# Kernel optimization log

Measured on AMD Instinct MI355X. Metric: run time of the kernel, lower is better.

The kernel has to match this reference:

```python
import jax, jax.numpy as jnp
import numpy as np

# Dims implied by init: input_dim=128, b_dim=64 -> per-branch Mamba d_model=16
D_MODEL = 16
D_STATE = 16
D_CONV = 4
D_INNER = 32   # expand * d_model
DT_RANK = 1    # ceil(d_model / 16)
EPS = 1e-5


def _ln(x, g, b):
    m = x.mean(-1, keepdims=True)
    v = x.var(-1, keepdims=True)
    return (x - m) / jnp.sqrt(v + EPS) * g + b


def _gn(x, g, b, groups):
    B, C, H, W = x.shape
    xr = x.reshape(B, groups, C // groups, H, W)
    m = xr.mean((2, 3, 4), keepdims=True)
    v = xr.var((2, 3, 4), keepdims=True)
    xr = (xr - m) / jnp.sqrt(v + EPS)
    return xr.reshape(B, C, H, W) * g[None, :, None, None] + b[None, :, None, None]


def _mamba(u, in_proj_w, conv_w, conv_b, x_proj_w, dt_proj_w, dt_proj_b, A_log, Dp, out_proj_w):
    # u: [N, L, d_model]
    N, L, _ = u.shape
    xz = u @ in_proj_w.T                       # [N, L, 2*d_inner]
    xc, zg = jnp.split(xz, 2, axis=-1)
    # causal depthwise conv1d over L
    xt = xc.transpose(0, 2, 1)                 # [N, d_inner, L]
    xt = jax.lax.conv_general_dilated(
        xt, conv_w, (1,), [(D_CONV - 1, 0)],
        dimension_numbers=('NCH', 'OIH', 'NCH'),
        feature_group_count=D_INNER)
    xt = xt + conv_b[None, :, None]
    xc = jax.nn.silu(xt).transpose(0, 2, 1)    # [N, L, d_inner]
    x_dbl = xc @ x_proj_w.T                    # [N, L, dt_rank + 2*d_state]
    dt = x_dbl[..., :DT_RANK]
    Bv = x_dbl[..., DT_RANK:DT_RANK + D_STATE]
    Cv = x_dbl[..., DT_RANK + D_STATE:]
    dt = jax.nn.softplus(dt @ dt_proj_w.T + dt_proj_b)  # [N, L, d_inner]
    A = -jnp.exp(A_log)                        # [d_inner, d_state]

    def step(h, inp):
        dt_t, B_t, C_t, x_t = inp              # [N,di],[N,ds],[N,ds],[N,di]
        dA = jnp.exp(dt_t[:, :, None] * A)     # [N, di, ds]
        h = dA * h + (dt_t * x_t)[:, :, None] * B_t[:, None, :]
        y = jnp.einsum('nds,ns->nd', h, C_t)
        return h, y

    h0 = jnp.zeros((N, D_INNER, D_STATE), u.dtype)
    xs = (dt.transpose(1, 0, 2), Bv.transpose(1, 0, 2),
          Cv.transpose(1, 0, 2), xc.transpose(1, 0, 2))
    _, ys = jax.lax.scan(step, h0, xs)         # ys: [L, N, d_inner]
    y = ys.transpose(1, 0, 2) + xc * Dp        # skip via D
    y = y * jax.nn.silu(zg)
    return y @ out_proj_w.T                    # [N, L, d_model]


def _forward(x, pre_ln_g, pre_ln_b, bott_in_w, bott_in_b,
             in_proj_w, conv_w, conv_b, x_proj_w, dt_proj_w, dt_proj_b,
             A_log, Dp, out_proj_w, post_ln_g, post_ln_b,
             bott_out_w, bott_out_b, res_scale,
             fc1_w, gn1_g, gn1_b, fc2_w, gn2_g, gn2_b):
    B, C, H, W = x.shape
    L = H * W
    # ---- PVMLayer token mixer ----
    xf = x.reshape(B, C, L).transpose(0, 2, 1)            # [B, L, C]
    z = _ln(xf, pre_ln_g, pre_ln_b)
    z = z @ bott_in_w.T + bott_in_b                       # [B, L, 64]
    # four chunks share the same Mamba weights -> batch them together
    zc = z.reshape(B, L, 4, D_MODEL).transpose(2, 0, 1, 3).reshape(4 * B, L, D_MODEL)
    m = _mamba(zc, in_proj_w, conv_w, conv_b, x_proj_w, dt_proj_w, dt_proj_b,
               A_log, Dp, out_proj_w) + zc
    z = m.reshape(4, B, L, D_MODEL).transpose(1, 2, 0, 3).reshape(B, L, 4 * D_MODEL)
    z = _ln(z, post_ln_g, post_ln_b)
    z = (z @ bott_out_w.T + bott_out_b) * res_scale       # [B, L, C]
    token = z.transpose(0, 2, 1).reshape(B, C, H, W)
    mixed = x + token                                     # PVMLayer residual (eval: drop_path=id)
    out = x + mixed                                       # PVMFormer residual
    # ---- Mlp (1x1 conv + GroupNorm) ----
    h = jnp.einsum('bchw,oc->bohw', out, fc1_w)
    h = _gn(h, gn1_g, gn1_b, 32)
    h = jax.nn.gelu(h, approximate=False)
    h = jnp.einsum('bchw,oc->bohw', h, fc2_w)
    h = _gn(h, gn2_g, gn2_b, 32)
    return out + h


def setup_inputs() -> dict:
    key = jax.random.key(0)
    ks = jax.random.split(key, 16)
    n = lambda k, s, sc=0.02: jax.random.normal(k, s, jnp.float32) * sc
    C = 128
    return {
        'x': jax.random.normal(ks[0], (8, C, 64, 64), jnp.float32),
        'pre_ln_g': jnp.ones((C,), jnp.float32),
        'pre_ln_b': jnp.zeros((C,), jnp.float32),
        'bott_in_w': n(ks[1], (64, C)),
        'bott_in_b': jnp.zeros((64,), jnp.float32),
        'in_proj_w': n(ks[2], (2 * D_INNER, D_MODEL)),
        'conv_w': n(ks[3], (D_INNER, 1, D_CONV), 0.1),
        'conv_b': jnp.zeros((D_INNER,), jnp.float32),
        'x_proj_w': n(ks[4], (DT_RANK + 2 * D_STATE, D_INNER)),
        'dt_proj_w': n(ks[5], (D_INNER, DT_RANK), 0.5),
        'dt_proj_b': n(ks[6], (D_INNER,), 0.5),
        'A_log': jnp.log(jnp.broadcast_to(jnp.arange(1.0, D_STATE + 1.0, dtype=jnp.float32), (D_INNER, D_STATE))),
        'Dp': jnp.ones((D_INNER,), jnp.float32),
        'out_proj_w': n(ks[7], (D_MODEL, D_INNER)),
        'post_ln_g': jnp.ones((64,), jnp.float32),
        'post_ln_b': jnp.zeros((64,), jnp.float32),
        'bott_out_w': n(ks[8], (C, 64)),
        'bott_out_b': jnp.zeros((C,), jnp.float32),
        'res_scale': jnp.array(0.5, jnp.float32),
        'fc1_w': n(ks[9], (4 * C, C)),
        'gn1_g': jnp.ones((4 * C,), jnp.float32),
        'gn1_b': jnp.zeros((4 * C,), jnp.float32),
        'fc2_w': n(ks[10], (C, 4 * C)),
        'gn2_g': jnp.ones((C,), jnp.float32),
        'gn2_b': jnp.zeros((C,), jnp.float32),
    }


def reference(x, pre_ln_g, pre_ln_b, bott_in_w, bott_in_b,
              in_proj_w, conv_w, conv_b, x_proj_w, dt_proj_w, dt_proj_b,
              A_log, Dp, out_proj_w, post_ln_g, post_ln_b,
              bott_out_w, bott_out_b, res_scale,
              fc1_w, gn1_g, gn1_b, fc2_w, gn2_g, gn2_b):
    return _forward(x, pre_ln_g, pre_ln_b, bott_in_w, bott_in_b,
                    in_proj_w, conv_w, conv_b, x_proj_w, dt_proj_w, dt_proj_b,
                    A_log, Dp, out_proj_w, post_ln_g, post_ln_b,
                    bott_out_w, bott_out_b, res_scale,
                    fc1_w, gn1_g, gn1_b, fc2_w, gn2_g, gn2_b)
```

## Files before the change

kernel.cpp:

```cpp
#include <hip/hip_runtime.h>
#include <hip/hip_bf16.h>
#include <math.h>

#define L4K 4096
#define NCH 32
#define CL  128
#define TB  32
#define NST (CL/TB)

typedef __attribute__((ext_vector_type(8))) short short8;
typedef __attribute__((ext_vector_type(4))) float f32x4;

__device__ __forceinline__ unsigned short f2b(float f) {
    unsigned int u = __float_as_uint(f);
    unsigned int r = u + 0x7FFFu + ((u >> 16) & 1u);
    return (unsigned short)(r >> 16);
}
__device__ __forceinline__ float b2f(unsigned short h) {
    return __uint_as_float(((unsigned int)h) << 16);
}

__global__ __launch_bounds__(256) void k1_pre(
    const float* __restrict__ x, const float* __restrict__ png, const float* __restrict__ pnb,
    const float* __restrict__ biw, const float* __restrict__ bib, const float* __restrict__ ipw,
    float* __restrict__ zc, float* __restrict__ xcp, float* __restrict__ zg)
{
    __shared__ float xs[128*32];
    __shared__ float wl[64*128];
    __shared__ float zs[32*65];
    __shared__ float ipl[64*16];
    __shared__ float pngs[128], pnbs[128];
    int tid = threadIdx.x;
    int l0 = blockIdx.x*32, b = blockIdx.y;
    const float* xb = x + (size_t)b*128*L4K;
    for (int it = 0; it < 16; ++it) {
        int f = it*256 + tid; int c = f>>5, i = f&31;
        xs[f] = xb[(size_t)c*L4K + l0 + i];
    }
    for (int f = tid; f < 8192; f += 256) wl[f] = biw[f];
    for (int f = tid; f < 1024; f += 256) ipl[f] = ipw[f];
    if (tid < 128) { pngs[tid] = png[tid]; pnbs[tid] = pnb[tid]; }
    __syncthreads();
    int i = tid & 31, q = tid >> 5;
    float s = 0.f, s2 = 0.f;
    for (int c = 0; c < 128; ++c) { float v = xs[c*32+i]; s += v; s2 = fmaf(v,v,s2); }
    float mn = s*(1.f/128.f);
    float rstd = rsqrtf(s2*(1.f/128.f) - mn*mn + 1e-5f);
    float z[8];
    #pragma unroll
    for (int jj = 0; jj < 8; ++jj) z[jj] = bib[q*8+jj];
    for (int c = 0; c < 128; ++c) {
        float xv = (xs[c*32+i] - mn)*rstd*pngs[c] + pnbs[c];
        #pragma unroll
        for (int jj = 0; jj < 8; ++jj) z[jj] = fmaf(xv, wl[(q*8+jj)*128 + c], z[jj]);
    }
    #pragma unroll
    for (int jj = 0; jj < 8; ++jj) zs[i*65 + q*8 + jj] = z[jj];
    __syncthreads();
    if (tid < 128) {
        int i2 = tid & 31, g = tid >> 5;
        int n = g*8 + b; int l = l0 + i2;
        float zv[16];
        #pragma unroll
        for (int k = 0; k < 16; ++k) zv[k] = zs[i2*65 + g*16 + k];
        size_t tb = (size_t)n*L4K + l;
        float4* zc4 = (float4*)(zc + tb*16);
        zc4[0] = make_float4(zv[0],zv[1],zv[2],zv[3]);
        zc4[1] = make_float4(zv[4],zv[5],zv[6],zv[7]);
        zc4[2] = make_float4(zv[8],zv[9],zv[10],zv[11]);
        zc4[3] = make_float4(zv[12],zv[13],zv[14],zv[15]);
        float* xo = xcp + tb*32;
        float* zo = zg + tb*32;
        #pragma unroll
        for (int o = 0; o < 64; ++o) {
            float a = 0.f;
            #pragma unroll
            for (int k = 0; k < 16; ++k) a = fmaf(zv[k], ipl[o*16+k], a);
            if (o < 32) xo[o] = a; else zo[o-32] = a;
        }
    }
}

__global__ __launch_bounds__(128) void k2_conv(
    const float* __restrict__ xcp, const float* __restrict__ cw, const float* __restrict__ cb,
    const float* __restrict__ xpw, const float* __restrict__ dtw, const float* __restrict__ dtb,
    float* __restrict__ S)
{
    __shared__ float xt[131*33];
    __shared__ float cwl[128], cbl[32], xpl[33*32], dtwl[32], dtbl[32];
    int tid = threadIdx.x;
    int t0 = blockIdx.x*128; int n = blockIdx.y;
    const float* xb = xcp + (size_t)n*L4K*32;
    for (int f = tid; f < 131*32; f += 128) {
        int r = f >> 5, d = f & 31;
        int t = t0 - 3 + r;
        xt[r*33 + d] = (t >= 0) ? xb[(size_t)t*32 + d] : 0.f;
    }
    if (tid < 128) cwl[tid] = cw[tid];
    if (tid < 32) { cbl[tid] = cb[tid]; dtwl[tid] = dtw[tid]; dtbl[tid] = dtb[tid]; }
    for (int f = tid; f < 33*32; f += 128) xpl[f] = xpw[f];
    __syncthreads();
    int t = t0 + tid;
    float xc[32];
    #pragma unroll
    for (int d = 0; d < 32; ++d) {
        float sv = cbl[d];
        #pragma unroll
        for (int k = 0; k < 4; ++k) sv = fmaf(cwl[d*4+k], xt[(tid+k)*33 + d], sv);
        xc[d] = sv / (1.f + __expf(-sv));
    }
    float dtr = 0.f; float Bv[16], Cv[16];
    #pragma unroll
    for (int dd = 0; dd < 32; ++dd) dtr = fmaf(xc[dd], xpl[dd], dtr);
    #pragma unroll
    for (int o = 0; o < 16; ++o) {
        float a = 0.f, a2 = 0.f;
        #pragma unroll
        for (int dd = 0; dd < 32; ++dd) {
            a  = fmaf(xc[dd], xpl[(1+o)*32+dd],  a);
            a2 = fmaf(xc[dd], xpl[(17+o)*32+dd], a2);
        }
        Bv[o] = a; Cv[o] = a2;
    }
    float* r = S + ((size_t)n*L4K + t)*128;
    #pragma unroll
    for (int d = 0; d < 32; ++d) {
        float dv = fmaf(dtr, dtwl[d], dtbl[d]);
        float sp = fmaxf(dv, 0.f) + log1pf(__expf(-fabsf(dv)));
        r[d]      = sp;
        r[32 + d] = sp * xc[d];
        r[96 + d] = xc[d];
    }
    #pragma unroll
    for (int o = 0; o < 16; ++o) { r[64+o] = Bv[o]; r[80+o] = Cv[o]; }
}

__global__ __launch_bounds__(512) void k3a_local(
    const float* __restrict__ S, const float* __restrict__ alog,
    float* __restrict__ chunkA, float* __restrict__ chunkH)
{
    __shared__ float sb[2][TB*128];
    int tid = threadIdx.x;
    int d = tid >> 4, s = tid & 15;
    int chunk = blockIdx.x, n = blockIdx.y;
    float A = -__expf(alog[d*16 + s]);
    const float4* Sg = (const float4*)(S + ((size_t)n*L4K + (size_t)chunk*CL)*128);
    float4 p0 = Sg[tid], p1 = Sg[tid + 512];
    ((float4*)sb[0])[tid] = p0; ((float4*)sb[0])[tid+512] = p1;
    __syncthreads();
    float h = 0.f, ap = 1.f;
    for (int st = 0; st < NST; ++st) {
        int cur = st & 1;
        float4 q0, q1;
        if (st+1 < NST) {
            const float4* Sn = Sg + (size_t)(st+1)*TB*32;
            q0 = Sn[tid]; q1 = Sn[tid+512];
        }
        const float* sc = sb[cur];
        #pragma unroll
        for (int tl = 0; tl < TB; ++tl) {
            float dtv = sc[tl*128 + d];
            float dxv = sc[tl*128 + 32 + d];
            float Bvv = sc[tl*128 + 64 + s];
            float dA = __expf(dtv * A);
            h = fmaf(dA, h, dxv * Bvv);
            ap *= dA;
        }
        if (st+1 < NST) {
            ((float4*)sb[cur^1])[tid] = q0;
            ((float4*)sb[cur^1])[tid+512] = q1;
            __syncthreads();
        }
    }
    chunkA[(size_t)chunk*16384 + n*512 + tid] = ap;
    chunkH[(size_t)chunk*16384 + n*512 + tid] = h;
}

__global__ __launch_bounds__(256) void k3b_prefix(
    const float* __restrict__ chunkA, const float* __restrict__ chunkH,
    float* __restrict__ hstart)
{
    int nds = blockIdx.x*256 + threadIdx.x;
    float h = 0.f;
    hstart[nds] = 0.f;
    for (int c = 0; c < NCH-1; ++c) {
        h = fmaf(h, chunkA[(size_t)c*16384 + nds], chunkH[(size_t)c*16384 + nds]);
        hstart[(size_t)(c+1)*16384 + nds] = h;
    }
}

__global__ __launch_bounds__(512) void k3c_emit(
    const float* __restrict__ S, const float* __restrict__ alog,
    const float* __restrict__ hstart, float* __restrict__ y)
{
    __shared__ float sb[2][TB*128];
    __shared__ float ys[TB*32];
    int tid = threadIdx.x;
    int d = tid >> 4, s = tid & 15;
    int chunk = blockIdx.x, n = blockIdx.y;
    float A = -__expf(alog[d*16 + s]);
    const float4* Sg = (const float4*)(S + ((size_t)n*L4K + (size_t)chunk*CL)*128);
    float4* yg = (float4*)(y + ((size_t)n*L4K + (size_t)chunk*CL)*32);
    float4 p0 = Sg[tid], p1 = Sg[tid + 512];
    ((float4*)sb[0])[tid] = p0; ((float4*)sb[0])[tid+512] = p1;
    float h = hstart[(size_t)chunk*16384 + n*512 + tid];
    __syncthreads();
    for (int st = 0; st < NST; ++st) {
        int cur = st & 1;
        float4 q0, q1;
        if (st+1 < NST) {
            const float4* Sn = Sg + (size_t)(st+1)*TB*32;
            q0 = Sn[tid]; q1 = Sn[tid+512];
        }
        const float* sc = sb[cur];
        #pragma unroll
        for (int tl = 0; tl < TB; ++tl) {
            float dtv = sc[tl*128 + d];
            float dxv = sc[tl*128 + 32 + d];
            float Bvv = sc[tl*128 + 64 + s];
            float Cvv = sc[tl*128 + 80 + s];
            float dA = __expf(dtv * A);
            h = fmaf(dA, h, dxv * Bvv);
            float p = h * Cvv;
            p += __shfl_xor(p, 8, 16);
            p += __shfl_xor(p, 4, 16);
            p += __shfl_xor(p, 2, 16);
            p += __shfl_xor(p, 1, 16);
            if (s == 0) ys[tl*32 + d] = p;
        }
        if (st+1 < NST) {
            ((float4*)sb[cur^1])[tid] = q0;
            ((float4*)sb[cur^1])[tid+512] = q1;
        }
        __syncthreads();
        if (tid < TB*8) yg[(size_t)st*TB*8 + tid] = ((const float4*)ys)[tid];
        __syncthreads();
    }
}

__global__ __launch_bounds__(256) void k5_out(
    const float* __restrict__ y, const float* __restrict__ S, const float* __restrict__ zg,
    const float* __restrict__ zc, const float* __restrict__ Dp, const float* __restrict__ opw,
    float* __restrict__ m)
{
    int id = blockIdx.x*256 + threadIdx.x;
    int n = id >> 12, t = id & 4095;
    const float* yp  = y  + (size_t)id*32;
    const float* xcr = S  + (size_t)id*128 + 96;
    const float* zgp = zg + (size_t)id*32;
    const float* zcp = zc + (size_t)id*16;
    float v[32];
    #pragma unroll
    for (int dd = 0; dd < 32; ++dd) {
        float g = zgp[dd];
        float sig = 1.f/(1.f + __expf(-g));
        v[dd] = (yp[dd] + xcr[dd]*Dp[dd]) * (g*sig);
    }
    int b = n & 7, g4 = n >> 3;
    float* mp = m + ((size_t)b*L4K + t)*64 + g4*16;
    #pragma unroll
    for (int j = 0; j < 16; ++j) {
        float a = zcp[j];
        #pragma unroll
        for (int dd = 0; dd < 32; ++dd) a = fmaf(v[dd], opw[j*32+dd], a);
        mp[j] = a;
    }
}

__global__ __launch_bounds__(256) void k6_post(
    const float* __restrict__ m, const float* __restrict__ x,
    const float* __restrict__ pog, const float* __restrict__ pob,
    const float* __restrict__ bow, const float* __restrict__ bob,
    const float* __restrict__ rsp, float* __restrict__ outp,
    unsigned short* __restrict__ outpb)
{
    __shared__ float ms[64*65];
    __shared__ float wl[128*64];
    __shared__ float pogs[64], pobs[64];
    int tid = threadIdx.x;
    int l0 = blockIdx.x*64, b = blockIdx.y;
    const float* mb = m + ((size_t)b*L4K + l0)*64;
    for (int f = tid; f < 4096; f += 256) {
        int i = f>>6, j = f&63;
        ms[i*65 + j] = mb[f];
    }
    for (int f = tid; f < 8192; f += 256) wl[f] = bow[f];
    if (tid < 64) { pogs[tid] = pog[tid]; pobs[tid] = pob[tid]; }
    __syncthreads();
    float rs = rsp[0];
    int i = tid & 63, q = tid >> 6;
    float s = 0.f, s2 = 0.f;
    for (int j = 0; j < 64; ++j) { float v = ms[i*65+j]; s += v; s2 = fmaf(v,v,s2); }
    float mn = s*(1.f/64.f);
    float rstd = rsqrtf(s2*(1.f/64.f) - mn*mn + 1e-5f);
    float acc[32];
    #pragma unroll
    for (int cc = 0; cc < 32; ++cc) acc[cc] = bob[q*32+cc];
    for (int j = 0; j < 64; ++j) {
        float v = (ms[i*65+j]-mn)*rstd*pogs[j] + pobs[j];
        #pragma unroll
        for (int cc = 0; cc < 32; ++cc) acc[cc] = fmaf(v, wl[(q*32+cc)*64+j], acc[cc]);
    }
    const float* xb = x + (size_t)b*128*L4K + l0 + i;
    float* ob = outp + (size_t)b*128*L4K + l0 + i;
    unsigned short pk[32];
    #pragma unroll
    for (int cc = 0; cc < 32; ++cc) {
        int c = q*32 + cc;
        float val = 2.f*xb[(size_t)c*L4K] + acc[cc]*rs;
        ob[(size_t)c*L4K] = val;
        pk[cc] = f2b(val);
    }
    uint4* op = (uint4*)&outpb[((size_t)b*L4K + l0 + i)*128 + q*32];
    #pragma unroll
    for (int u = 0; u < 4; ++u) {
        uint4 v;
        v.x = pk[u*8+0] | ((unsigned)pk[u*8+1]<<16);
        v.y = pk[u*8+2] | ((unsigned)pk[u*8+3]<<16);
        v.z = pk[u*8+4] | ((unsigned)pk[u*8+5]<<16);
        v.w = pk[u*8+6] | ((unsigned)pk[u*8+7]<<16);
        op[u] = v;
    }
}

template<int KCHUNKS, bool OUT_BF16>
__global__ __launch_bounds__(256) void gemm_mfma(
    const unsigned short* __restrict__ Ab, const float* __restrict__ Wg,
    void* __restrict__ Dout, int Kpitch, int Npitch)
{
    __shared__ char lds[65536];
    int tid = threadIdx.x;
    int lane = tid & 63, w = tid >> 6;
    int l0 = blockIdx.x * 128, n0 = blockIdx.y * 128, b = blockIdx.z;
    size_t arow0 = (size_t)b*L4K + l0;
    int wm = (w>>1)*64, wn = (w&1)*64;
    f32x4 acc[4][4] = {};
    char* aL = lds;
    char* wL = lds + 32768;
    for (int kc = 0; kc < KCHUNKS; ++kc) {
        if (kc) __syncthreads();
        #pragma unroll
        for (int it = 0; it < 8; ++it) {
            int f = it*256 + tid;
            int row = f >> 4, kp = f & 15;
            uint4 v = *(const uint4*)&Ab[(arow0 + row)*(size_t)Kpitch + kc*128 + kp*8];
            int off = row*256 + kp*16; off ^= (row&7)<<4;
            *(uint4*)(aL + off) = v;
        }
        #pragma unroll
        for (int it = 0; it < 16; ++it) {
            int f = it*256 + tid;
            int row = f >> 5, kg = f & 31;
            float4 v = *(const float4*)&Wg[(size_t)(n0+row)*(KCHUNKS*128) + kc*128 + kg*4];
            uint2 p;
            p.x = f2b(v.x) | ((unsigned)f2b(v.y)<<16);
            p.y = f2b(v.z) | ((unsigned)f2b(v.w)<<16);
            int off = row*256 + kg*8; off ^= (row&7)<<4;
            *(uint2*)(wL + off) = p;
        }
        __syncthreads();
        #pragma unroll
        for (int ks = 0; ks < 4; ++ks) {
            short8 af[4], wf[4];
            int kb = ks*64 + (lane>>4)*16;
            #pragma unroll
            for (int mi = 0; mi < 4; ++mi) {
                int row = wm + mi*16 + (lane&15);
                int off = row*256 + kb; off ^= (row&7)<<4;
                af[mi] = *(const short8*)(aL + off);
            }
            #pragma unroll
            for (int ni = 0; ni < 4; ++ni) {
                int row = wn + ni*16 + (lane&15);
                int off = row*256 + kb; off ^= (row&7)<<4;
                wf[ni] = *(const short8*)(wL + off);
            }
            #pragma unroll
            for (int mi = 0; mi < 4; ++mi)
                #pragma unroll
                for (int ni = 0; ni < 4; ++ni)
                    acc[mi][ni] = __builtin_amdgcn_mfma_f32_16x16x32_bf16(af[mi], wf[ni], acc[mi][ni], 0, 0, 0);
        }
    }
    if (OUT_BF16) {
        __syncthreads();
        unsigned short* cL = (unsigned short*)lds;
        #pragma unroll
        for (int mi = 0; mi < 4; ++mi)
            #pragma unroll
            for (int ni = 0; ni < 4; ++ni)
                #pragma unroll
                for (int r = 0; r < 4; ++r) {
                    int row = wm + mi*16 + (lane>>4)*4 + r;
                    int col = wn + ni*16 + (lane&15);
                    cL[row*136 + col] = f2b(acc[mi][ni][r]);
                }
        __syncthreads();
        unsigned short* D = (unsigned short*)Dout;
        #pragma unroll
        for (int it = 0; it < 8; ++it) {
            int f = it*256 + tid;
            int row = f >> 4, kp = f & 15;
            uint4 v = *(const uint4*)&cL[row*136 + kp*8];
            *(uint4*)&D[(arow0 + row)*(size_t)Npitch + n0 + kp*8] = v;
        }
    } else {
        float* D = (float*)Dout;
        #pragma unroll
        for (int mi = 0; mi < 4; ++mi)
            #pragma unroll
            for (int ni = 0; ni < 4; ++ni)
                #pragma unroll
                for (int r = 0; r < 4; ++r) {
                    int row = wm + mi*16 + (lane>>4)*4 + r;
                    int col = wn + ni*16 + (lane&15);
                    D[(arow0 + row)*(size_t)Npitch + n0 + col] = acc[mi][ni][r];
                }
    }
}

__global__ __launch_bounds__(256) void k_gn1stats(
    const unsigned short* __restrict__ h, float* __restrict__ stats)
{
    __shared__ float sred[256], sred2[256];
    int tid = threadIdx.x;
    int b = blockIdx.x >> 5, g = blockIdx.x & 31;
    float s = 0.f, s2 = 0.f;
    for (int it = 0; it < 32; ++it) {
        int f = it*256 + tid;
        int l = f >> 1, half = f & 1;
        uint4 v = *(const uint4*)&h[((size_t)b*L4K + l)*512 + g*16 + half*8];
        unsigned int ws[4] = {v.x, v.y, v.z, v.w};
        #pragma unroll
        for (int u = 0; u < 4; ++u) {
            float a = b2f((unsigned short)(ws[u] & 0xFFFF));
            float c = b2f((unsigned short)(ws[u] >> 16));
            s += a + c; s2 = fmaf(a,a,s2); s2 = fmaf(c,c,s2);
        }
    }
    sred[tid] = s; sred2[tid] = s2; __syncthreads();
    for (int off = 128; off; off >>= 1) {
        if (tid < off) { sred[tid] += sred[tid+off]; sred2[tid] += sred2[tid+off]; }
        __syncthreads();
    }
    if (tid == 0) {
        float inv = 1.f/65536.f;
        float mn = sred[0]*inv;
        float var = sred2[0]*inv - mn*mn;
        stats[blockIdx.x*2]   = mn;
        stats[blockIdx.x*2+1] = rsqrtf(var + 1e-5f);
    }
}

__global__ __launch_bounds__(256) void k9_gngelu(
    unsigned short* __restrict__ h, const float* __restrict__ stats,
    const float* __restrict__ g1, const float* __restrict__ b1)
{
    size_t idx = ((size_t)blockIdx.x*256 + threadIdx.x)*8;
    int o0 = (int)(idx & 511);
    int b = (int)(idx >> 21);
    int sg = b*32 + (o0 >> 4);
    float mn = stats[sg*2], rstd = stats[sg*2+1];
    uint4 v = *(uint4*)&h[idx];
    unsigned int ws[4] = {v.x, v.y, v.z, v.w};
    unsigned int out[4];
    #pragma unroll
    for (int u = 0; u < 4; ++u) {
        float a = b2f((unsigned short)(ws[u] & 0xFFFF));
        float c = b2f((unsigned short)(ws[u] >> 16));
        int o = o0 + u*2;
        float ta = (a-mn)*rstd*g1[o]   + b1[o];
        float tc = (c-mn)*rstd*g1[o+1] + b1[o+1];
        ta = 0.5f*ta*(1.f + erff(ta*0.70710678118654752f));
        tc = 0.5f*tc*(1.f + erff(tc*0.70710678118654752f));
        out[u] = f2b(ta) | ((unsigned)f2b(tc)<<16);
    }
    uint4 r; r.x = out[0]; r.y = out[1]; r.z = out[2]; r.w = out[3];
    *(uint4*)&h[idx] = r;
}

__global__ __launch_bounds__(256) void k_gn2stats(
    const float* __restrict__ h, float* __restrict__ stats)
{
    __shared__ float sred[256], sred2[256];
    int tid = threadIdx.x;
    int b = blockIdx.x >> 5, g = blockIdx.x & 31;
    float s = 0.f, s2 = 0.f;
    for (int it = 0; it < 16; ++it) {
        int l = it*256 + tid;
        float4 v = ((const float4*)h)[((size_t)b*L4K + l)*32 + g];
        s += v.x+v.y+v.z+v.w;
        s2 = fmaf(v.x,v.x,s2); s2 = fmaf(v.y,v.y,s2); s2 = fmaf(v.z,v.z,s2); s2 = fmaf(v.w,v.w,s2);
    }
    sred[tid] = s; sred2[tid] = s2; __syncthreads();
    for (int off = 128; off; off >>= 1) {
        if (tid < off) { sred[tid] += sred[tid+off]; sred2[tid] += sred2[tid+off]; }
        __syncthreads();
    }
    if (tid == 0) {
        float inv = 1.f/16384.f;
        float mn = sred[0]*inv;
        float var = sred2[0]*inv - mn*mn;
        stats[blockIdx.x*2]   = mn;
        stats[blockIdx.x*2+1] = rsqrtf(var + 1e-5f);
    }
}

__global__ __launch_bounds__(256) void k12_final(
    const float* __restrict__ outp, const float* __restrict__ h2t,
    const float* __restrict__ stats, const float* __restrict__ g2,
    const float* __restrict__ b2, float* __restrict__ out)
{
    __shared__ float T[32*33];
    int tid = threadIdx.x;
    int l0 = blockIdx.x*32, c0 = blockIdx.y*32, b = blockIdx.z;
    {
        int i = tid >> 3, jq = tid & 7;
        float4 v = ((const float4*)h2t)[((size_t)b*L4K + l0 + i)*32 + (c0>>2) + jq];
        int sg = b*32 + (c0>>2) + jq;
        float mn = stats[sg*2], rstd = stats[sg*2+1];
        int c = c0 + jq*4;
        T[(jq*4+0)*33 + i] = (v.x-mn)*rstd*g2[c+0] + b2[c+0];
        T[(jq*4+1)*33 + i] = (v.y-mn)*rstd*g2[c+1] + b2[c+1];
        T[(jq*4+2)*33 + i] = (v.z-mn)*rstd*g2[c+2] + b2[c+2];
        T[(jq*4+3)*33 + i] = (v.w-mn)*rstd*g2[c+3] + b2[c+3];
    }
    __syncthreads();
    {
        int c = tid >> 3, iq = tid & 7;
        size_t gi = ((size_t)b*128 + c0 + c)*1024 + (l0>>2) + iq;
        float4 o = ((const float4*)outp)[gi];
        float4 r;
        r.x = o.x + T[c*33 + iq*4 + 0];
        r.y = o.y + T[c*33 + iq*4 + 1];
        r.z = o.z + T[c*33 + iq*4 + 2];
        r.w = o.w + T[c*33 + iq*4 + 3];
        ((float4*)out)[gi] = r;
    }
}

extern "C" void kernel_launch(void* const* d_in, const int* in_sizes, int n_in,
                              void* d_out, int out_size, void* d_ws, size_t ws_size,
                              hipStream_t stream) {
    (void)in_sizes; (void)n_in; (void)out_size; (void)ws_size;
    const float* x    = (const float*)d_in[0];
    const float* png  = (const float*)d_in[1];
    const float* pnb  = (const float*)d_in[2];
    const float* biw  = (const float*)d_in[3];
    const float* bib  = (const float*)d_in[4];
    const float* ipw  = (const float*)d_in[5];
    const float* cw   = (const float*)d_in[6];
    const float* cb   = (const float*)d_in[7];
    const float* xpw  = (const float*)d_in[8];
    const float* dtw  = (const float*)d_in[9];
    const float* dtb  = (const float*)d_in[10];
    const float* alog = (const float*)d_in[11];
    const float* Dp   = (const float*)d_in[12];
    const float* opw  = (const float*)d_in[13];
    const float* pog  = (const float*)d_in[14];
    const float* pob  = (const float*)d_in[15];
    const float* bow  = (const float*)d_in[16];
    const float* bob  = (const float*)d_in[17];
    const float* rsp  = (const float*)d_in[18];
    const float* f1w  = (const float*)d_in[19];
    const float* g1g  = (const float*)d_in[20];
    const float* g1b  = (const float*)d_in[21];
    const float* f2w  = (const float*)d_in[22];
    const float* g2g  = (const float*)d_in[23];
    const float* g2b  = (const float*)d_in[24];

    char* ws = (char*)d_ws;
    float* S    = (float*)(ws + 0);
    float* zc   = (float*)(ws + 67108864);
    float* zg   = (float*)(ws + 75497472);
    float* xcp  = (float*)(ws + 92274688);
    float* y    = (float*)(ws + 92274688);
    float* m    = (float*)(ws + 109051904);
    float* chA  = (float*)(ws + 109051904);
    float* chH  = (float*)(ws + 109051904 + 2097152);
    float* hst  = (float*)(ws + 109051904 + 4194304);
    float*          outp  = (float*)(ws + 0);
    unsigned short* outpb = (unsigned short*)(ws + 16777216);
    unsigned short* h1tb  = (unsigned short*)(ws + 25165824);
    float*          h2t   = (float*)(ws + 58720256);
    float*          st1   = (float*)(ws + 75497472);
    float*          st2   = (float*)(ws + 75501568);

    k1_pre<<<dim3(128,8),256,0,stream>>>(x,png,pnb,biw,bib,ipw,zc,xcp,zg);
    k2_conv<<<dim3(32,32),128,0,stream>>>(xcp,cw,cb,xpw,dtw,dtb,S);
    k3a_local<<<dim3(NCH,32),512,0,stream>>>(S,alog,chA,chH);
    k3b_prefix<<<64,256,0,stream>>>(chA,chH,hst);
    k3c_emit<<<dim3(NCH,32),512,0,stream>>>(S,alog,hst,y);
    k5_out<<<512,256,0,stream>>>(y,S,zg,zc,Dp,opw,m);
    k6_post<<<dim3(64,8),256,0,stream>>>(m,x,pog,pob,bow,bob,rsp,outp,outpb);
    gemm_mfma<1,true><<<dim3(32,4,8),256,0,stream>>>(outpb,f1w,(void*)h1tb,128,512);
    k_gn1stats<<<256,256,0,stream>>>(h1tb,st1);
    k9_gngelu<<<8192,256,0,stream>>>(h1tb,st1,g1g,g1b);
    gemm_mfma<4,false><<<dim3(32,1,8),256,0,stream>>>(h1tb,f2w,(void*)h2t,512,128);
    k_gn2stats<<<256,256,0,stream>>>(h2t,st2);
    k12_final<<<dim3(128,4,8),256,0,stream>>>(outp,h2t,st2,g2g,g2b,(float*)d_out);
}
```

Baseline: 476.5 us.

## Switch intermediates to channel-major layout and stream scan inputs from global memory

Intermediate buffers (zc, xcp, zg, S, y, m) are stored channel-major, [n][channel][time], instead of time-major, so per-thread time-indexed accesses coalesce across threads. The chunked scan kernels drop their LDS double-buffering and instead read float4 runs of time steps directly from global memory, with a one-step register prefetch. The emit kernel replaces its shuffle reduction with a DPP row reduction and writes y straight out. The risk is that each thread now streams its own strided rows, relying on cache hits for the redundant B/C reads across d, and that k1's scattered writes become more strided.

```diff
diff --git a/kernel.cpp b/kernel.cpp
--- a/kernel.cpp
+++ b/kernel.cpp
@@ -5,8 +5,7 @@
 #define L4K 4096
 #define NCH 32
 #define CL  128
-#define TB  32
-#define NST (CL/TB)
+#define SPN (128*4096)
 
 typedef __attribute__((ext_vector_type(8))) short short8;
 typedef __attribute__((ext_vector_type(4))) float f32x4;
@@ -18,6 +17,18 @@
 }
 __device__ __forceinline__ float b2f(unsigned short h) {
     return __uint_as_float(((unsigned int)h) << 16);
+}
+__device__ __forceinline__ float rowsum16(float p) {
+    int t;
+    t = __builtin_amdgcn_update_dpp(0, __float_as_int(p), 0x128, 0xf, 0xf, false);
+    p += __int_as_float(t);
+    t = __builtin_amdgcn_update_dpp(0, __float_as_int(p), 0x124, 0xf, 0xf, false);
+    p += __int_as_float(t);
+    t = __builtin_amdgcn_update_dpp(0, __float_as_int(p), 0x122, 0xf, 0xf, false);
+    p += __int_as_float(t);
+    t = __builtin_amdgcn_update_dpp(0, __float_as_int(p), 0x121, 0xf, 0xf, false);
+    p += __int_as_float(t);
+    return p;
 }
 
 __global__ __launch_bounds__(256) void k1_pre(
@@ -63,20 +74,17 @@
         float zv[16];
         #pragma unroll
         for (int k = 0; k < 16; ++k) zv[k] = zs[i2*65 + g*16 + k];
-        size_t tb = (size_t)n*L4K + l;
-        float4* zc4 = (float4*)(zc + tb*16);
-        zc4[0] = make_float4(zv[0],zv[1],zv[2],zv[3]);
-        zc4[1] = make_float4(zv[4],zv[5],zv[6],zv[7]);
-        zc4[2] = make_float4(zv[8],zv[9],zv[10],zv[11]);
-        zc4[3] = make_float4(zv[12],zv[13],zv[14],zv[15]);
-        float* xo = xcp + tb*32;
-        float* zo = zg + tb*32;
+        float* zcb = zc + ((size_t)n*16)*L4K + l;
+        #pragma unroll
+        for (int k = 0; k < 16; ++k) zcb[(size_t)k*L4K] = zv[k];
+        float* xo = xcp + ((size_t)n*32)*L4K + l;
+        float* zo = zg  + ((size_t)n*32)*L4K + l;
         #pragma unroll
         for (int o = 0; o < 64; ++o) {
             float a = 0.f;
             #pragma unroll
             for (int k = 0; k < 16; ++k) a = fmaf(zv[k], ipl[o*16+k], a);
-            if (o < 32) xo[o] = a; else zo[o-32] = a;
+            if (o < 32) xo[(size_t)o*L4K] = a; else zo[(size_t)(o-32)*L4K] = a;
         }
     }
 }
@@ -90,11 +98,15 @@
     __shared__ float cwl[128], cbl[32], xpl[33*32], dtwl[32], dtbl[32];
     int tid = threadIdx.x;
     int t0 = blockIdx.x*128; int n = blockIdx.y;
-    const float* xb = xcp + (size_t)n*L4K*32;
-    for (int f = tid; f < 131*32; f += 128) {
-        int r = f >> 5, d = f & 31;
-        int t = t0 - 3 + r;
-        xt[r*33 + d] = (t >= 0) ? xb[(size_t)t*32 + d] : 0.f;
+    const float* xb = xcp + (size_t)n*32*L4K;
+    #pragma unroll 4
+    for (int d = 0; d < 32; ++d) {
+        int t = t0 - 3 + tid;
+        xt[tid*33 + d] = (t >= 0) ? xb[(size_t)d*L4K + t] : 0.f;
+        if (tid < 3) {
+            int r = 128 + tid; int t2 = t0 - 3 + r;
+            xt[r*33 + d] = xb[(size_t)d*L4K + t2];
+        }
     }
     if (tid < 128) cwl[tid] = cw[tid];
     if (tid < 32) { cbl[tid] = cb[tid]; dtwl[tid] = dtw[tid]; dtbl[tid] = dtb[tid]; }
@@ -122,58 +134,49 @@
         }
         Bv[o] = a; Cv[o] = a2;
     }
-    float* r = S + ((size_t)n*L4K + t)*128;
+    float* Sn = S + (size_t)n*SPN + t;
     #pragma unroll
     for (int d = 0; d < 32; ++d) {
         float dv = fmaf(dtr, dtwl[d], dtbl[d]);
         float sp = fmaxf(dv, 0.f) + log1pf(__expf(-fabsf(dv)));
-        r[d]      = sp;
-        r[32 + d] = sp * xc[d];
-        r[96 + d] = xc[d];
-    }
-    #pragma unroll
-    for (int o = 0; o < 16; ++o) { r[64+o] = Bv[o]; r[80+o] = Cv[o]; }
+        Sn[(size_t)d*L4K]      = sp;
+        Sn[(size_t)(32+d)*L4K] = sp * xc[d];
+        Sn[(size_t)(96+d)*L4K] = xc[d];
+    }
+    #pragma unroll
+    for (int o = 0; o < 16; ++o) {
+        Sn[(size_t)(64+o)*L4K] = Bv[o];
+        Sn[(size_t)(80+o)*L4K] = Cv[o];
+    }
 }
 
 __global__ __launch_bounds__(512) void k3a_local(
     const float* __restrict__ S, const float* __restrict__ alog,
     float* __restrict__ chunkA, float* __restrict__ chunkH)
 {
-    __shared__ float sb[2][TB*128];
     int tid = threadIdx.x;
     int d = tid >> 4, s = tid & 15;
     int chunk = blockIdx.x, n = blockIdx.y;
     float A = -__expf(alog[d*16 + s]);
-    const float4* Sg = (const float4*)(S + ((size_t)n*L4K + (size_t)chunk*CL)*128);
-    float4 p0 = Sg[tid], p1 = Sg[tid + 512];
-    ((float4*)sb[0])[tid] = p0; ((float4*)sb[0])[tid+512] = p1;
-    __syncthreads();
+    const float* base = S + (size_t)n*SPN + (size_t)chunk*CL;
+    const float4* pdt = (const float4*)(base + (size_t)d*L4K);
+    const float4* pdx = (const float4*)(base + (size_t)(32+d)*L4K);
+    const float4* pB  = (const float4*)(base + (size_t)(64+s)*L4K);
+    float4 cdt = pdt[0], cdx = pdx[0], cB = pB[0];
     float h = 0.f, ap = 1.f;
-    for (int st = 0; st < NST; ++st) {
-        int cur = st & 1;
-        float4 q0, q1;
-        if (st+1 < NST) {
-            const float4* Sn = Sg + (size_t)(st+1)*TB*32;
-            q0 = Sn[tid]; q1 = Sn[tid+512];
-        }
-        const float* sc = sb[cur];
-        #pragma unroll
-        for (int tl = 0; tl < TB; ++tl) {
-            float dtv = sc[tl*128 + d];
-            float dxv = sc[tl*128 + 32 + d];
-            float Bvv = sc[tl*128 + 64 + s];
-            float dA = __expf(dtv * A);
-            h = fmaf(dA, h, dxv * Bvv);
-            ap *= dA;
-        }
-        if (st+1 < NST) {
-            ((float4*)sb[cur^1])[tid] = q0;
-            ((float4*)sb[cur^1])[tid+512] = q1;
-            __syncthreads();
-        }
-    }
-    chunkA[(size_t)chunk*16384 + n*512 + tid] = ap;
-    chunkH[(size_t)chunk*16384 + n*512 + tid] = h;
+    #define A_STEP(c1,c2,c3) { float dA = __expf(c1*A); h = fmaf(dA, h, c2*c3); ap *= dA; }
+    for (int i = 0; i < CL/4 - 1; ++i) {
+        float4 ndt = pdt[i+1], ndx = pdx[i+1], nB = pB[i+1];
+        A_STEP(cdt.x, cdx.x, cB.x) A_STEP(cdt.y, cdx.y, cB.y)
+        A_STEP(cdt.z, cdx.z, cB.z) A_STEP(cdt.w, cdx.w, cB.w)
+        cdt = ndt; cdx = ndx; cB = nB;
+    }
+    A_STEP(cdt.x, cdx.x, cB.x) A_STEP(cdt.y, cdx.y, cB.y)
+    A_STEP(cdt.z, cdx.z, cB.z) A_STEP(cdt.w, cdx.w, cB.w)
+    #undef A_STEP
+    size_t idx = (size_t)chunk*16384 + n*512 + tid;
+    chunkA[idx] = ap;
+    chunkH[idx] = h;
 }
 
 __global__ __launch_bounds__(256) void k3b_prefix(
@@ -193,49 +196,38 @@
     const float* __restrict__ S, const float* __restrict__ alog,
     const float* __restrict__ hstart, float* __restrict__ y)
 {
-    __shared__ float sb[2][TB*128];
-    __shared__ float ys[TB*32];
     int tid = threadIdx.x;
     int d = tid >> 4, s = tid & 15;
     int chunk = blockIdx.x, n = blockIdx.y;
     float A = -__expf(alog[d*16 + s]);
-    const float4* Sg = (const float4*)(S + ((size_t)n*L4K + (size_t)chunk*CL)*128);
-    float4* yg = (float4*)(y + ((size_t)n*L4K + (size_t)chunk*CL)*32);
-    float4 p0 = Sg[tid], p1 = Sg[tid + 512];
-    ((float4*)sb[0])[tid] = p0; ((float4*)sb[0])[tid+512] = p1;
+    const float* base = S + (size_t)n*SPN + (size_t)chunk*CL;
+    const float4* pdt = (const float4*)(base + (size_t)d*L4K);
+    const float4* pdx = (const float4*)(base + (size_t)(32+d)*L4K);
+    const float4* pB  = (const float4*)(base + (size_t)(64+s)*L4K);
+    const float4* pC  = (const float4*)(base + (size_t)(80+s)*L4K);
+    float4* yb = (float4*)(y + ((size_t)n*32 + d)*L4K + (size_t)chunk*CL);
+    float4 cdt = pdt[0], cdx = pdx[0], cB = pB[0], cC = pC[0];
     float h = hstart[(size_t)chunk*16384 + n*512 + tid];
-    __syncthreads();
-    for (int st = 0; st < NST; ++st) {
-        int cur = st & 1;
-        float4 q0, q1;
-        if (st+1 < NST) {
-            const float4* Sn = Sg + (size_t)(st+1)*TB*32;
-            q0 = Sn[tid]; q1 = Sn[tid+512];
-        }
-        const float* sc = sb[cur];
-        #pragma unroll
-        for (int tl = 0; tl < TB; ++tl) {
-            float dtv = sc[tl*128 + d];
-            float dxv = sc[tl*128 + 32 + d];
-            float Bvv = sc[tl*128 + 64 + s];
-            float Cvv = sc[tl*128 + 80 + s];
-            float dA = __expf(dtv * A);
-            h = fmaf(dA, h, dxv * Bvv);
-            float p = h * Cvv;
-            p += __shfl_xor(p, 8, 16);
-            p += __shfl_xor(p, 4, 16);
-            p += __shfl_xor(p, 2, 16);
-            p += __shfl_xor(p, 1, 16);
-            if (s == 0) ys[tl*32 + d] = p;
-        }
-        if (st+1 < NST) {
-            ((float4*)sb[cur^1])[tid] = q0;
-            ((float4*)sb[cur^1])[tid+512] = q1;
-        }
-        __syncthreads();
-        if (tid < TB*8) yg[(size_t)st*TB*8 + tid] = ((const float4*)ys)[tid];
-        __syncthreads();
-    }
+    #define C_STEP(c1,c2,c3,c4,dst) { float dA = __expf(c1*A); h = fmaf(dA, h, c2*c3); dst = rowsum16(h*c4); }
+    for (int i = 0; i < CL/4 - 1; ++i) {
+        float4 ndt = pdt[i+1], ndx = pdx[i+1], nB = pB[i+1], nC = pC[i+1];
+        float4 yv;
+        C_STEP(cdt.x, cdx.x, cB.x, cC.x, yv.x)
+        C_STEP(cdt.y, cdx.y, cB.y, cC.y, yv.y)
+        C_STEP(cdt.z, cdx.z, cB.z, cC.z, yv.z)
+        C_STEP(cdt.w, cdx.w, cB.w, cC.w, yv.w)
+        if (s == 0) yb[i] = yv;
+        cdt = ndt; cdx = ndx; cB = nB; cC = nC;
+    }
+    {
+        float4 yv;
+        C_STEP(cdt.x, cdx.x, cB.x, cC.x, yv.x)
+        C_STEP(cdt.y, cdx.y, cB.y, cC.y, yv.y)
+        C_STEP(cdt.z, cdx.z, cB.z, cC.z, yv.z)
+        C_STEP(cdt.w, cdx.w, cB.w, cC.w, yv.w)
+        if (s == 0) yb[CL/4 - 1] = yv;
+    }
+    #undef C_STEP
 }
 
 __global__ __launch_bounds__(256) void k5_out(
@@ -245,25 +237,25 @@
 {
     int id = blockIdx.x*256 + threadIdx.x;
     int n = id >> 12, t = id & 4095;
-    const float* yp  = y  + (size_t)id*32;
-    const float* xcr = S  + (size_t)id*128 + 96;
-    const float* zgp = zg + (size_t)id*32;
-    const float* zcp = zc + (size_t)id*16;
+    const float* yb  = y  + (size_t)n*32*L4K + t;
+    const float* xcb = S  + (size_t)n*SPN + (size_t)96*L4K + t;
+    const float* zgb = zg + (size_t)n*32*L4K + t;
+    const float* zcb = zc + (size_t)n*16*L4K + t;
     float v[32];
     #pragma unroll
     for (int dd = 0; dd < 32; ++dd) {
-        float g = zgp[dd];
+        float g = zgb[(size_t)dd*L4K];
         float sig = 1.f/(1.f + __expf(-g));
-        v[dd] = (yp[dd] + xcr[dd]*Dp[dd]) * (g*sig);
+        v[dd] = (yb[(size_t)dd*L4K] + xcb[(size_t)dd*L4K]*Dp[dd]) * (g*sig);
     }
     int b = n & 7, g4 = n >> 3;
-    float* mp = m + ((size_t)b*L4K + t)*64 + g4*16;
+    float* mp = m + ((size_t)b*64 + g4*16)*L4K + t;
     #pragma unroll
     for (int j = 0; j < 16; ++j) {
-        float a = zcp[j];
+        float a = zcb[(size_t)j*L4K];
         #pragma unroll
         for (int dd = 0; dd < 32; ++dd) a = fmaf(v[dd], opw[j*32+dd], a);
-        mp[j] = a;
+        mp[(size_t)j*L4K] = a;
     }
 }
 
@@ -279,10 +271,9 @@
     __shared__ float pogs[64], pobs[64];
     int tid = threadIdx.x;
     int l0 = blockIdx.x*64, b = blockIdx.y;
-    const float* mb = m + ((size_t)b*L4K + l0)*64;
     for (int f = tid; f < 4096; f += 256) {
-        int i = f>>6, j = f&63;
-        ms[i*65 + j] = mb[f];
+        int i = f & 63, j = f >> 6;
+        ms[i*65 + j] = m[((size_t)b*64 + j)*L4K + l0 + i];
     }
     for (int f = tid; f < 8192; f += 256) wl[f] = bow[f];
     if (tid < 64) { pogs[tid] = pog[tid]; pobs[tid] = pob[tid]; }
```

Measured after the change: 460.1 us. 1.04x faster.
